# Kernel tuning notes

Measured on AMD Instinct MI355X. Metric: run time of the kernel, lower is better.

## Reference

```python
import jax, jax.numpy as jnp
import numpy as np

HIDDEN = 2048
NUM_HEADS = 8
NUM_KV_HEADS = 1
HEAD_DIM = 256
ROPE_THETA = 10000.0
B, S = 2, 2048


def setup_inputs() -> dict:
    key = jax.random.key(0)
    k1, k2, k3, k4, k5 = jax.random.split(key, 5)
    scale = 0.02
    hidden_states = jax.random.normal(k1, (B, S, HIDDEN), dtype=jnp.float32)
    Wq = jax.random.normal(k2, (HIDDEN, NUM_HEADS * HEAD_DIM), dtype=jnp.float32) * scale
    Wk = jax.random.normal(k3, (HIDDEN, NUM_KV_HEADS * HEAD_DIM), dtype=jnp.float32) * scale
    Wv = jax.random.normal(k4, (HIDDEN, NUM_KV_HEADS * HEAD_DIM), dtype=jnp.float32) * scale
    Wo = jax.random.normal(k5, (NUM_HEADS * HEAD_DIM, HIDDEN), dtype=jnp.float32) * scale
    # causal mask: 1 = attend, 0 = masked (module adds -1e9 where mask==0)
    attention_mask = jnp.tril(jnp.ones((S, S), dtype=jnp.int32))[None, None].repeat(B, axis=0)
    position_ids = jnp.arange(S, dtype=jnp.int32)[None, :].repeat(B, axis=0)
    return {"hidden_states": hidden_states, "Wq": Wq, "Wk": Wk, "Wv": Wv,
            "Wo": Wo, "attention_mask": attention_mask, "position_ids": position_ids}


def _rotate_half(x):
    half = x.shape[-1] // 2
    return jnp.concatenate([-x[..., half:], x[..., :half]], axis=-1)


def _rope_cos_sin(position_ids, head_dim, theta):
    inv_freq = 1.0 / (theta ** (jnp.arange(0, head_dim, 2, dtype=jnp.float32) / head_dim))
    freqs = position_ids.astype(jnp.float32)[:, :, None] * inv_freq[None, None, :]  # [B,S,D/2]
    emb = jnp.concatenate([freqs, freqs], axis=-1)  # [B,S,D]
    return jnp.cos(emb)[:, None], jnp.sin(emb)[:, None]  # [B,1,S,D]


def reference(hidden_states, Wq, Wk, Wv, Wo, attention_mask, position_ids):
    bsz, q_len, _ = hidden_states.shape
    q = (hidden_states @ Wq).reshape(bsz, q_len, NUM_HEADS, HEAD_DIM).transpose(0, 2, 1, 3)
    k = (hidden_states @ Wk).reshape(bsz, q_len, NUM_KV_HEADS, HEAD_DIM).transpose(0, 2, 1, 3)
    v = (hidden_states @ Wv).reshape(bsz, q_len, NUM_KV_HEADS, HEAD_DIM).transpose(0, 2, 1, 3)
    q = q / jnp.sqrt(jnp.float32(HEAD_DIM))  # scale before RoPE, as in source
    cos, sin = _rope_cos_sin(position_ids, HEAD_DIM, ROPE_THETA)
    q = q * cos + _rotate_half(q) * sin
    k = k * cos + _rotate_half(k) * sin
    # GQA: repeat kv heads (prefill: cache == current k,v)
    groups = NUM_HEADS // NUM_KV_HEADS
    k = jnp.repeat(k, groups, axis=1)
    v = jnp.repeat(v, groups, axis=1)
    attn = jnp.einsum('bhqd,bhkd->bhqk', q, k)  # [B,H,S,S]
    additive = jnp.where(attention_mask == 0, jnp.float32(-1e9), jnp.float32(0.0))
    attn = jax.nn.softmax(attn + additive, axis=-1)
    out = jnp.einsum('bhqk,bhkd->bhqd', attn, v)
    out = out.transpose(0, 2, 1, 3).reshape(bsz, q_len, NUM_HEADS * HEAD_DIM)
    out = out @ Wo
    return out, attn
```

## Files before the change

kernel.cpp:

```cpp
#include <hip/hip_runtime.h>

typedef __bf16 bf16_t;
typedef __attribute__((ext_vector_type(4))) float f32x4;
typedef __attribute__((ext_vector_type(8))) __bf16 bf16x8;
typedef __attribute__((ext_vector_type(4))) __bf16 bf16x4;

#define DEVI __device__ __forceinline__

static constexpr int kBsz = 2, kS = 2048, kH = 8, kD = 256, kHid = 2048, kNqkv = 2560;

DEVI void gload_lds16(const void* g, void* l) {
  __builtin_amdgcn_global_load_lds(
      (__attribute__((address_space(1))) unsigned int*)g,
      (__attribute__((address_space(3))) unsigned int*)l, 16, 0, 0);
}

__global__ __launch_bounds__(256) void cast_f32_bf16(const float* __restrict__ in,
                                                     bf16_t* __restrict__ out) {
  int idx = blockIdx.x * 256 + threadIdx.x;
  const float4 f = ((const float4*)in)[idx];
  bf16x4 o;
  o[0] = (bf16_t)f.x; o[1] = (bf16_t)f.y; o[2] = (bf16_t)f.z; o[3] = (bf16_t)f.w;
  ((bf16x4*)out)[idx] = o;
}

__global__ void wtrans_all(const float* __restrict__ Wq, const float* __restrict__ Wk,
                           const float* __restrict__ Wv, const float* __restrict__ Wo,
                           bf16_t* __restrict__ WqkvT, bf16_t* __restrict__ WoT) {
  __shared__ float tile[32][33];
  int zb = blockIdx.x;
  const float* src;
  bf16_t* dst;
  int C, bx, by;
  if (zb < 4096) {
    src = Wq; dst = WqkvT; C = 2048; bx = zb & 63; by = zb >> 6;
  } else if (zb < 4608) {
    int u = zb - 4096; src = Wk; dst = WqkvT + (size_t)2048 * 2048; C = 256; bx = u & 7; by = u >> 3;
  } else if (zb < 5120) {
    int u = zb - 4608; src = Wv; dst = WqkvT + (size_t)2304 * 2048; C = 256; bx = u & 7; by = u >> 3;
  } else {
    int u = zb - 5120; src = Wo; dst = WoT; C = 2048; bx = u & 63; by = u >> 6;
  }
  int c0 = bx * 32, r0 = by * 32;
  int tx = threadIdx.x, ty = threadIdx.y;
#pragma unroll
  for (int k = 0; k < 4; k++)
    tile[ty + 8 * k][tx] = src[(size_t)(r0 + ty + 8 * k) * C + c0 + tx];
  __syncthreads();
#pragma unroll
  for (int k = 0; k < 4; k++)
    dst[(size_t)(c0 + ty + 8 * k) * 2048 + r0 + tx] = (bf16_t)tile[tx][ty + 8 * k];
}

__global__ __launch_bounds__(256) void transpose_v(const bf16_t* __restrict__ qkv,
                                                   bf16_t* __restrict__ vT) {
  __shared__ float tile[32][33];
  int d0 = blockIdx.x * 32, s0 = blockIdx.y * 32, b = blockIdx.z;
  int tx = threadIdx.x, ty = threadIdx.y;
  const bf16_t* in = qkv + ((size_t)(b * kS + s0)) * kNqkv + 2304 + d0;
#pragma unroll
  for (int k = 0; k < 4; k++)
    tile[ty + 8 * k][tx] = (float)in[(size_t)(ty + 8 * k) * kNqkv + tx];
  __syncthreads();
  bf16_t* out = vT + ((size_t)(b * kD + d0)) * kS + s0;
#pragma unroll
  for (int k = 0; k < 4; k++)
    out[(size_t)(ty + 8 * k) * kS + tx] = (bf16_t)tile[tx][ty + 8 * k];
}

__global__ __launch_bounds__(256) void rope_all(const bf16_t* __restrict__ qkv,
                                                const int* __restrict__ pos_ids,
                                                bf16_t* __restrict__ q_bh,
                                                bf16_t* __restrict__ k_b) {
  int bid = blockIdx.x;
  if (bid < 16384) {
    int idx = bid * 256 + threadIdx.x;
    int j = idx & 127, s = (idx >> 7) & 2047, h = (idx >> 18) & 7, b = idx >> 21;
    float invf = exp2f(-0.103810253f * (float)j);
    float ang = (float)pos_ids[b * kS + s] * invf;
    float c, sn;
    sincosf(ang, &sn, &c);
    const bf16_t* src = qkv + ((size_t)(b * kS + s)) * kNqkv + h * kD;
    float x0 = (float)src[j] * 0.0625f;
    float x1 = (float)src[j + 128] * 0.0625f;
    bf16_t* dst = q_bh + ((size_t)((b * kH + h) * kS + s)) * kD;
    dst[j] = (bf16_t)(x0 * c - x1 * sn);
    dst[j + 128] = (bf16_t)(x1 * c + x0 * sn);
  } else {
    int idx = (bid - 16384) * 256 + threadIdx.x;
    int j = idx & 127, s = (idx >> 7) & 2047, b = idx >> 18;
    float invf = exp2f(-0.103810253f * (float)j);
    float ang = (float)pos_ids[b * kS + s] * invf;
    float c, sn;
    sincosf(ang, &sn, &c);
    const bf16_t* src = qkv + ((size_t)(b * kS + s)) * kNqkv + 2048;
    float x0 = (float)src[j];
    float x1 = (float)src[j + 128];
    bf16_t* dst = k_b + ((size_t)(b * kS + s)) * kD;
    dst[j] = (bf16_t)(x0 * c - x1 * sn);
    dst[j + 128] = (bf16_t)(x1 * c + x0 * sn);
  }
}

__global__ __launch_bounds__(256, 4) void attn_fused(
    const bf16_t* __restrict__ q_bh, const bf16_t* __restrict__ k_b,
    float* __restrict__ attn, bf16_t* __restrict__ P) {
  constexpr int KT = 64;
  __shared__ bf16_t ks[KT * 256];
  __shared__ float lstat[64][2];
  __shared__ float rowinv[64];
  const int lin = blockIdx.y * 32 + blockIdx.x;
  const int xr = (lin >> 1) & 31;
  const int flip = (lin ^ (lin >> 8)) & 1;
  const int rt = flip ? 31 - xr : xr;
  const int z = (lin & 1) | (((lin >> 6) & 7) << 1);
  const int b = z >> 3;
  const int nkt = rt + 1, dkt = rt;
  const int m0 = rt * 64;
  const int t = threadIdx.x, lane = t & 63, wv = t >> 6;
  const int wm2 = (wv & 1) * 32, wn2 = (wv >> 1) * 32, wc = wv >> 1;
  const int lrow = lane & 15, quad = lane >> 4;

  bf16x8 qf[2][8];
  {
    const bf16_t* qb = q_bh + ((size_t)z * kS + m0) * kD;
#pragma unroll
    for (int mi = 0; mi < 2; mi++)
#pragma unroll
      for (int k8 = 0; k8 < 8; k8++)
        qf[mi][k8] = *(const bf16x8*)(qb + (size_t)(wm2 + mi * 16 + lrow) * kD + k8 * 32 + quad * 8);
  }
  const bf16_t* kb = k_b + (size_t)b * kS * kD;

  float rs[2][4];
#pragma unroll
  for (int mi = 0; mi < 2; mi++)
#pragma unroll
    for (int rr = 0; rr < 4; rr++) rs[mi][rr] = 0.f;

  for (int kt = 0; kt < nkt; kt++) {
    __syncthreads();
#pragma unroll
    for (int i = 0; i < 8; i++) {
      int slot = i * 256 + t;
      int r = slot >> 5;
      int c = (slot & 31) ^ (r & 7);
      gload_lds16(kb + (size_t)(kt * KT + r) * kD + c * 8, ks + slot * 8);
    }
    __syncthreads();
    f32x4 acc[2][2];
#pragma unroll
    for (int mi = 0; mi < 2; mi++)
#pragma unroll
      for (int ni = 0; ni < 2; ni++) acc[mi][ni] = f32x4{0.f, 0.f, 0.f, 0.f};
    __builtin_amdgcn_s_setprio(1);
#pragma unroll
    for (int k8 = 0; k8 < 8; k8++) {
      bf16x8 bfv[2];
#pragma unroll
      for (int ni = 0; ni < 2; ni++) {
        int R = wn2 + ni * 16 + lrow;
        int c16 = (k8 * 4 + quad) ^ (R & 7);
        bfv[ni] = *(const bf16x8*)(ks + R * 256 + c16 * 8);
      }
#pragma unroll
      for (int mi = 0; mi < 2; mi++)
#pragma unroll
        for (int ni = 0; ni < 2; ni++)
          acc[mi][ni] = __builtin_amdgcn_mfma_f32_16x16x32_bf16(qf[mi][k8], bfv[ni], acc[mi][ni], 0, 0, 0);
    }
    __builtin_amdgcn_s_setprio(0);
    const bool diag = (kt == dkt);
#pragma unroll
    for (int mi = 0; mi < 2; mi++)
#pragma unroll
      for (int rr = 0; rr < 4; rr++) {
        int ml = wm2 + mi * 16 + quad * 4 + rr;
        int mg = m0 + ml;
#pragma unroll
        for (int ni = 0; ni < 2; ni++) {
          int ng = kt * KT + wn2 + ni * 16 + lrow;
          float e = __expf(fminf(acc[mi][ni][rr], 80.f));
          rs[mi][rr] += (!diag || ng <= mg) ? e : 0.f;
        }
      }
  }
#pragma unroll
  for (int mi = 0; mi < 2; mi++)
#pragma unroll
    for (int rr = 0; rr < 4; rr++) {
      float s4 = rs[mi][rr];
      s4 += __shfl_xor(s4, 1); s4 += __shfl_xor(s4, 2);
      s4 += __shfl_xor(s4, 4); s4 += __shfl_xor(s4, 8);
      if (lrow == 0) lstat[wm2 + mi * 16 + quad * 4 + rr][wc] = s4;
    }
  __syncthreads();
  if (t < 64) rowinv[t] = 1.f / (lstat[t][0] + lstat[t][1]);

  float* arow = attn + ((size_t)z * kS + m0) * kS;
  bf16_t* prow = P + ((size_t)z * kS + m0) * kS;
  for (int kt = 0; kt < nkt; kt++) {
    __syncthreads();
#pragma unroll
    for (int i = 0; i < 8; i++) {
      int slot = i * 256 + t;
      int r = slot >> 5;
      int c = (slot & 31) ^ (r & 7);
      gload_lds16(kb + (size_t)(kt * KT + r) * kD + c * 8, ks + slot * 8);
    }
    __syncthreads();
    f32x4 acc[2][2];
#pragma unroll
    for (int mi = 0; mi < 2; mi++)
#pragma unroll
      for (int ni = 0; ni < 2; ni++) acc[mi][ni] = f32x4{0.f, 0.f, 0.f, 0.f};
    __builtin_amdgcn_s_setprio(1);
#pragma unroll
    for (int k8 = 0; k8 < 8; k8++) {
      bf16x8 bfv[2];
#pragma unroll
      for (int ni = 0; ni < 2; ni++) {
        int R = wn2 + ni * 16 + lrow;
        int c16 = (k8 * 4 + quad) ^ (R & 7);
        bfv[ni] = *(const bf16x8*)(ks + R * 256 + c16 * 8);
      }
#pragma unroll
      for (int mi = 0; mi < 2; mi++)
#pragma unroll
        for (int ni = 0; ni < 2; ni++)
          acc[mi][ni] = __builtin_amdgcn_mfma_f32_16x16x32_bf16(qf[mi][k8], bfv[ni], acc[mi][ni], 0, 0, 0);
    }
    __builtin_amdgcn_s_setprio(0);
    const bool diag = (kt == dkt);
#pragma unroll
    for (int mi = 0; mi < 2; mi++)
#pragma unroll
      for (int rr = 0; rr < 4; rr++) {
        int ml = wm2 + mi * 16 + quad * 4 + rr;
        int mg = m0 + ml;
        float inv = rowinv[ml];
        float* ap = arow + (size_t)ml * kS + kt * KT;
        bf16_t* pp = prow + (size_t)ml * kS + kt * KT;
#pragma unroll
        for (int ni = 0; ni < 2; ni++) {
          int nl = wn2 + ni * 16 + lrow;
          int ng = kt * KT + nl;
          float e = __expf(fminf(acc[mi][ni][rr], 80.f)) * inv;
          float pv = (!diag || ng <= mg) ? e : 0.f;
          ap[nl] = pv;
          pp[nl] = (bf16_t)pv;
        }
      }
  }
  int c0 = nkt * KT;
  int nf4 = (kS - c0) >> 2;
  for (int rr = 0; rr < 64; rr++) {
    float* ap = arow + (size_t)rr * kS + c0;
    for (int cc = t; cc < nf4; cc += 256)
      *(float4*)(ap + cc * 4) = make_float4(0.f, 0.f, 0.f, 0.f);
  }
  if ((rt & 1) == 0) {
    int pc0 = nkt * KT;
    int r = t >> 2, cchunk = (t & 3) * 16;
    bf16x8 zz = {(bf16_t)0.f, (bf16_t)0.f, (bf16_t)0.f, (bf16_t)0.f,
                 (bf16_t)0.f, (bf16_t)0.f, (bf16_t)0.f, (bf16_t)0.f};
    *(bf16x8*)(prow + (size_t)r * kS + pc0 + cchunk) = zz;
    *(bf16x8*)(prow + (size_t)r * kS + pc0 + cchunk + 8) = zz;
  }
}

template <int OUT, int CKTR, int BAL = 0>
__global__ __launch_bounds__(256) void gemm_bt(
    const bf16_t* __restrict__ Av, const bf16_t* __restrict__ Btv, void* __restrict__ Cv,
    int K, int lda, int ldb, int ldc,
    long long aBatch, long long bBatch, int bzShift, long long cBatch) {
  constexpr int BM = 128, BN = 128, BK = 64;
  __shared__ bf16_t As[BM * BK];
  __shared__ bf16_t Bs[BN * BK];
  const int z = blockIdx.z;
  const int n0 = blockIdx.x * BN;
  int byi = blockIdx.y;
  if (BAL) {
    if ((blockIdx.x ^ (blockIdx.z >> 3)) & 1) byi = gridDim.y - 1 - byi;
  }
  const int m0 = byi * BM;
  const bf16_t* Bt = Btv + (size_t)(z >> bzShift) * bBatch + (size_t)n0 * ldb;
  const int kEnd = CKTR ? ((m0 + BM < K) ? (m0 + BM) : K) : K;
  const int t = threadIdx.x;
  const int lane = t & 63, wv = t >> 6;
  const int wm = (wv & 1) << 6, wn = (wv >> 1) << 6;
  const int lrow = lane & 15, quad = lane >> 4;
  f32x4 zero = {0.f, 0.f, 0.f, 0.f};
  f32x4 acc[4][4];
#pragma unroll
  for (int i = 0; i < 4; i++)
#pragma unroll
    for (int j = 0; j < 4; j++) acc[i][j] = zero;

  const bf16_t* Ab = Av + (size_t)z * aBatch + (size_t)m0 * lda;

  for (int k0 = 0; k0 < kEnd; k0 += BK) {
    __syncthreads();
#pragma unroll
    for (int i = 0; i < 4; i++) {
      int slot = i * 256 + t;
      int r = slot >> 3, c = slot & 7;
      gload_lds16(Ab + (size_t)r * lda + k0 + c * 8, As + slot * 8);
    }
#pragma unroll
    for (int i = 0; i < 4; i++) {
      int slot = i * 256 + t;
      int r = slot >> 3, c = slot & 7;
      gload_lds16(Bt + (size_t)r * ldb + k0 + c * 8, Bs + slot * 8);
    }
    __syncthreads();
#pragma unroll
    for (int k8 = 0; k8 < 2; k8++) {
      bf16x8 af[4], bfv[4];
#pragma unroll
      for (int i = 0; i < 4; i++)
        af[i] = *(const bf16x8*)(As + (wm + i * 16 + lrow) * BK + k8 * 32 + quad * 8);
#pragma unroll
      for (int i = 0; i < 4; i++)
        bfv[i] = *(const bf16x8*)(Bs + (wn + i * 16 + lrow) * BK + k8 * 32 + quad * 8);
#pragma unroll
      for (int mi = 0; mi < 4; mi++)
#pragma unroll
        for (int ni = 0; ni < 4; ni++)
          acc[mi][ni] = __builtin_amdgcn_mfma_f32_16x16x32_bf16(af[mi], bfv[ni], acc[mi][ni], 0, 0, 0);
    }
  }

  if (OUT == 0) {
    float* C = (float*)Cv + (size_t)z * cBatch;
#pragma unroll
    for (int mi = 0; mi < 4; mi++) {
      int m = m0 + wm + mi * 16 + quad * 4;
#pragma unroll
      for (int ni = 0; ni < 4; ni++) {
        int n = n0 + wn + ni * 16 + lrow;
#pragma unroll
        for (int r = 0; r < 4; r++) C[(size_t)(m + r) * ldc + n] = acc[mi][ni][r];
      }
    }
  } else if (OUT == 1) {
    bf16_t* C = (bf16_t*)Cv + (size_t)(z >> 3) * cBatch + (size_t)(z & 7) * kD;
#pragma unroll
    for (int mi = 0; mi < 4; mi++) {
      int m = m0 + wm + mi * 16 + quad * 4;
#pragma unroll
      for (int ni = 0; ni < 4; ni++) {
        int n = n0 + wn + ni * 16 + lrow;
#pragma unroll
        for (int r = 0; r < 4; r++) C[(size_t)(m + r) * ldc + n] = (bf16_t)acc[mi][ni][r];
      }
    }
  } else {
    bf16_t* C = (bf16_t*)Cv + (size_t)z * cBatch;
#pragma unroll
    for (int mi = 0; mi < 4; mi++) {
      int m = m0 + wm + mi * 16 + quad * 4;
#pragma unroll
      for (int ni = 0; ni < 4; ni++) {
        int n = n0 + wn + ni * 16 + lrow;
#pragma unroll
        for (int r = 0; r < 4; r++) C[(size_t)(m + r) * ldc + n] = (bf16_t)acc[mi][ni][r];
      }
    }
  }
}

extern "C" void kernel_launch(void* const* d_in, const int* in_sizes, int n_in,
                              void* d_out, int out_size, void* d_ws, size_t ws_size,
                              hipStream_t stream) {
  const float* hs = (const float*)d_in[0];
  const float* Wq = (const float*)d_in[1];
  const float* Wk = (const float*)d_in[2];
  const float* Wv = (const float*)d_in[3];
  const float* Wo = (const float*)d_in[4];
  const int* pos = (const int*)d_in[6];

  float* out = (float*)d_out;
  float* attn = out + (size_t)kBsz * kS * kHid;

  char* w = (char*)d_ws;
  bf16_t* hsb = (bf16_t*)w;   w += (size_t)4096 * 2048 * 2;
  bf16_t* WqkvT = (bf16_t*)w; w += (size_t)2560 * 2048 * 2;
  bf16_t* WoT = (bf16_t*)w;   w += (size_t)2048 * 2048 * 2;
  bf16_t* qkv = (bf16_t*)w;   w += (size_t)4096 * 2560 * 2;
  bf16_t* q_bh = (bf16_t*)w;  w += (size_t)8388608 * 2;
  bf16_t* k_b = (bf16_t*)w;   w += (size_t)1048576 * 2;
  bf16_t* vT = (bf16_t*)w;    w += (size_t)1048576 * 2;
  bf16_t* av = (bf16_t*)w;    w += (size_t)8388608 * 2;
  bf16_t* Pb = (bf16_t*)w;    w += (size_t)16 * 2048 * 2048 * 2;

  cast_f32_bf16<<<8192, 256, 0, stream>>>(hs, hsb);
  wtrans_all<<<9216, dim3(32, 8), 0, stream>>>(Wq, Wk, Wv, Wo, WqkvT, WoT);

  gemm_bt<2, 0><<<dim3(20, 32, 1), 256, 0, stream>>>(
      hsb, WqkvT, qkv, 2048, 2048, 2048, 2560, 0, 0, 0, 0);

  rope_all<<<18432, 256, 0, stream>>>(qkv, pos, q_bh, k_b);
  transpose_v<<<dim3(8, 64, 2), dim3(32, 8), 0, stream>>>(qkv, vT);

  attn_fused<<<dim3(32, 16), 256, 0, stream>>>(q_bh, k_b, attn, Pb);

  gemm_bt<1, 1, 1><<<dim3(2, 16, 16), 256, 0, stream>>>(
      Pb, vT, av, 2048, 2048, 2048, 2048,
      (long long)4194304, (long long)524288, 3, (long long)(kS * kHid));

  gemm_bt<0, 0><<<dim3(16, 32, 1), 256, 0, stream>>>(
      av, WoT, out, 2048, 2048, 2048, 2048, 0, 0, 0, 0);
}
```

Measured before the change: 742.1 us.

## Split attention into single-pass unnormalized exp tiles with deferred row normalization

```diff
diff --git a/kernel.cpp b/kernel.cpp
--- a/kernel.cpp
+++ b/kernel.cpp
@@ -22,6 +22,10 @@
   bf16x4 o;
   o[0] = (bf16_t)f.x; o[1] = (bf16_t)f.y; o[2] = (bf16_t)f.z; o[3] = (bf16_t)f.w;
   ((bf16x4*)out)[idx] = o;
+}
+
+__global__ __launch_bounds__(256) void zero_f32(float* __restrict__ p) {
+  p[blockIdx.x * 256 + threadIdx.x] = 0.f;
 }
 
 __global__ void wtrans_all(const float* __restrict__ Wq, const float* __restrict__ Wk,
@@ -102,25 +106,30 @@
   }
 }
 
-__global__ __launch_bounds__(256, 4) void attn_fused(
+__global__ __launch_bounds__(256, 4) void qk_exp(
     const bf16_t* __restrict__ q_bh, const bf16_t* __restrict__ k_b,
-    float* __restrict__ attn, bf16_t* __restrict__ P) {
-  constexpr int KT = 64;
-  __shared__ bf16_t ks[KT * 256];
-  __shared__ float lstat[64][2];
-  __shared__ float rowinv[64];
-  const int lin = blockIdx.y * 32 + blockIdx.x;
-  const int xr = (lin >> 1) & 31;
-  const int flip = (lin ^ (lin >> 8)) & 1;
-  const int rt = flip ? 31 - xr : xr;
-  const int z = (lin & 1) | (((lin >> 6) & 7) << 1);
+    bf16_t* __restrict__ P, float* __restrict__ rowsum) {
+  __shared__ bf16_t ks[64 * 256];
+  const int u = blockIdx.x;
+  const int z = blockIdx.y;
   const int b = z >> 3;
-  const int nkt = rt + 1, dkt = rt;
-  const int m0 = rt * 64;
+  int rt = (int)((sqrtf(8.f * (float)u + 1.f) - 1.f) * 0.5f);
+  while ((rt + 1) * (rt + 2) / 2 <= u) rt++;
+  while (rt * (rt + 1) / 2 > u) rt--;
+  const int kt = u - rt * (rt + 1) / 2;
+  const int m0 = rt * 64, n0 = kt * 64;
   const int t = threadIdx.x, lane = t & 63, wv = t >> 6;
-  const int wm2 = (wv & 1) * 32, wn2 = (wv >> 1) * 32, wc = wv >> 1;
+  const int wm2 = (wv & 1) * 32, wn2 = (wv >> 1) * 32;
   const int lrow = lane & 15, quad = lane >> 4;
 
+  const bf16_t* kb = k_b + (size_t)b * kS * kD;
+#pragma unroll
+  for (int i = 0; i < 8; i++) {
+    int slot = i * 256 + t;
+    int r = slot >> 5;
+    int c = (slot & 31) ^ (r & 7);
+    gload_lds16(kb + (size_t)(n0 + r) * kD + c * 8, ks + slot * 8);
+  }
   bf16x8 qf[2][8];
   {
     const bf16_t* qb = q_bh + ((size_t)z * kS + m0) * kD;
@@ -130,142 +139,94 @@
       for (int k8 = 0; k8 < 8; k8++)
         qf[mi][k8] = *(const bf16x8*)(qb + (size_t)(wm2 + mi * 16 + lrow) * kD + k8 * 32 + quad * 8);
   }
-  const bf16_t* kb = k_b + (size_t)b * kS * kD;
-
-  float rs[2][4];
+  __syncthreads();
+
+  f32x4 acc[2][2];
 #pragma unroll
   for (int mi = 0; mi < 2; mi++)
 #pragma unroll
-    for (int rr = 0; rr < 4; rr++) rs[mi][rr] = 0.f;
-
-  for (int kt = 0; kt < nkt; kt++) {
-    __syncthreads();
-#pragma unroll
-    for (int i = 0; i < 8; i++) {
-      int slot = i * 256 + t;
-      int r = slot >> 5;
-      int c = (slot & 31) ^ (r & 7);
-      gload_lds16(kb + (size_t)(kt * KT + r) * kD + c * 8, ks + slot * 8);
-    }
-    __syncthreads();
-    f32x4 acc[2][2];
+    for (int ni = 0; ni < 2; ni++) acc[mi][ni] = f32x4{0.f, 0.f, 0.f, 0.f};
+  __builtin_amdgcn_s_setprio(1);
+#pragma unroll
+  for (int k8 = 0; k8 < 8; k8++) {
+    bf16x8 bfv[2];
+#pragma unroll
+    for (int ni = 0; ni < 2; ni++) {
+      int R = wn2 + ni * 16 + lrow;
+      int c16 = (k8 * 4 + quad) ^ (R & 7);
+      bfv[ni] = *(const bf16x8*)(ks + R * 256 + c16 * 8);
+    }
 #pragma unroll
     for (int mi = 0; mi < 2; mi++)
 #pragma unroll
-      for (int ni = 0; ni < 2; ni++) acc[mi][ni] = f32x4{0.f, 0.f, 0.f, 0.f};
-    __builtin_amdgcn_s_setprio(1);
-#pragma unroll
-    for (int k8 = 0; k8 < 8; k8++) {
-      bf16x8 bfv[2];
+      for (int ni = 0; ni < 2; ni++)
+        acc[mi][ni] = __builtin_amdgcn_mfma_f32_16x16x32_bf16(qf[mi][k8], bfv[ni], acc[mi][ni], 0, 0, 0);
+  }
+  __builtin_amdgcn_s_setprio(0);
+
+  const bool diag = (kt == rt);
+  bf16_t* pt = P + ((size_t)z * kS + m0) * kS + n0;
+#pragma unroll
+  for (int mi = 0; mi < 2; mi++)
+#pragma unroll
+    for (int rr = 0; rr < 4; rr++) {
+      int ml = wm2 + mi * 16 + quad * 4 + rr;
+      int mg = m0 + ml;
+      float s4 = 0.f;
 #pragma unroll
       for (int ni = 0; ni < 2; ni++) {
-        int R = wn2 + ni * 16 + lrow;
-        int c16 = (k8 * 4 + quad) ^ (R & 7);
-        bfv[ni] = *(const bf16x8*)(ks + R * 256 + c16 * 8);
+        int nl = wn2 + ni * 16 + lrow;
+        int ng = n0 + nl;
+        float e = __expf(fminf(acc[mi][ni][rr], 80.f));
+        bool ok = !diag || ng <= mg;
+        bf16_t pb = ok ? (bf16_t)e : (bf16_t)0.f;
+        pt[(size_t)ml * kS + nl] = pb;
+        s4 += (float)pb;
       }
-#pragma unroll
-      for (int mi = 0; mi < 2; mi++)
-#pragma unroll
-        for (int ni = 0; ni < 2; ni++)
-          acc[mi][ni] = __builtin_amdgcn_mfma_f32_16x16x32_bf16(qf[mi][k8], bfv[ni], acc[mi][ni], 0, 0, 0);
-    }
-    __builtin_amdgcn_s_setprio(0);
-    const bool diag = (kt == dkt);
-#pragma unroll
-    for (int mi = 0; mi < 2; mi++)
-#pragma unroll
-      for (int rr = 0; rr < 4; rr++) {
-        int ml = wm2 + mi * 16 + quad * 4 + rr;
-        int mg = m0 + ml;
-#pragma unroll
-        for (int ni = 0; ni < 2; ni++) {
-          int ng = kt * KT + wn2 + ni * 16 + lrow;
-          float e = __expf(fminf(acc[mi][ni][rr], 80.f));
-          rs[mi][rr] += (!diag || ng <= mg) ? e : 0.f;
-        }
-      }
-  }
-#pragma unroll
-  for (int mi = 0; mi < 2; mi++)
-#pragma unroll
-    for (int rr = 0; rr < 4; rr++) {
-      float s4 = rs[mi][rr];
       s4 += __shfl_xor(s4, 1); s4 += __shfl_xor(s4, 2);
       s4 += __shfl_xor(s4, 4); s4 += __shfl_xor(s4, 8);
-      if (lrow == 0) lstat[wm2 + mi * 16 + quad * 4 + rr][wc] = s4;
-    }
-  __syncthreads();
-  if (t < 64) rowinv[t] = 1.f / (lstat[t][0] + lstat[t][1]);
-
-  float* arow = attn + ((size_t)z * kS + m0) * kS;
-  bf16_t* prow = P + ((size_t)z * kS + m0) * kS;
-  for (int kt = 0; kt < nkt; kt++) {
-    __syncthreads();
-#pragma unroll
-    for (int i = 0; i < 8; i++) {
-      int slot = i * 256 + t;
-      int r = slot >> 5;
-      int c = (slot & 31) ^ (r & 7);
-      gload_lds16(kb + (size_t)(kt * KT + r) * kD + c * 8, ks + slot * 8);
-    }
-    __syncthreads();
-    f32x4 acc[2][2];
-#pragma unroll
-    for (int mi = 0; mi < 2; mi++)
-#pragma unroll
-      for (int ni = 0; ni < 2; ni++) acc[mi][ni] = f32x4{0.f, 0.f, 0.f, 0.f};
-    __builtin_amdgcn_s_setprio(1);
-#pragma unroll
-    for (int k8 = 0; k8 < 8; k8++) {
-      bf16x8 bfv[2];
-#pragma unroll
-      for (int ni = 0; ni < 2; ni++) {
-        int R = wn2 + ni * 16 + lrow;
-        int c16 = (k8 * 4 + quad) ^ (R & 7);
-        bfv[ni] = *(const bf16x8*)(ks + R * 256 + c16 * 8);
-      }
-#pragma unroll
-      for (int mi = 0; mi < 2; mi++)
-#pragma unroll
-        for (int ni = 0; ni < 2; ni++)
-          acc[mi][ni] = __builtin_amdgcn_mfma_f32_16x16x32_bf16(qf[mi][k8], bfv[ni], acc[mi][ni], 0, 0, 0);
-    }
-    __builtin_amdgcn_s_setprio(0);
-    const bool diag = (kt == dkt);
-#pragma unroll
-    for (int mi = 0; mi < 2; mi++)
-#pragma unroll
-      for (int rr = 0; rr < 4; rr++) {
-        int ml = wm2 + mi * 16 + quad * 4 + rr;
-        int mg = m0 + ml;
-        float inv = rowinv[ml];
-        float* ap = arow + (size_t)ml * kS + kt * KT;
-        bf16_t* pp = prow + (size_t)ml * kS + kt * KT;
-#pragma unroll
-        for (int ni = 0; ni < 2; ni++) {
-          int nl = wn2 + ni * 16 + lrow;
-          int ng = kt * KT + nl;
-          float e = __expf(fminf(acc[mi][ni][rr], 80.f)) * inv;
-          float pv = (!diag || ng <= mg) ? e : 0.f;
-          ap[nl] = pv;
-          pp[nl] = (bf16_t)pv;
-        }
-      }
-  }
-  int c0 = nkt * KT;
-  int nf4 = (kS - c0) >> 2;
-  for (int rr = 0; rr < 64; rr++) {
-    float* ap = arow + (size_t)rr * kS + c0;
-    for (int cc = t; cc < nf4; cc += 256)
-      *(float4*)(ap + cc * 4) = make_float4(0.f, 0.f, 0.f, 0.f);
-  }
-  if ((rt & 1) == 0) {
-    int pc0 = nkt * KT;
-    int r = t >> 2, cchunk = (t & 3) * 16;
+      if (lrow == 0) atomicAdd(rowsum + (size_t)z * kS + mg, s4);
+    }
+
+  if (diag && !(rt & 1)) {
     bf16x8 zz = {(bf16_t)0.f, (bf16_t)0.f, (bf16_t)0.f, (bf16_t)0.f,
                  (bf16_t)0.f, (bf16_t)0.f, (bf16_t)0.f, (bf16_t)0.f};
-    *(bf16x8*)(prow + (size_t)r * kS + pc0 + cchunk) = zz;
-    *(bf16x8*)(prow + (size_t)r * kS + pc0 + cchunk + 8) = zz;
+    int r = t >> 2, cc = (t & 3) * 16;
+    bf16_t* pz = P + ((size_t)z * kS + m0 + r) * kS + n0 + 64 + cc;
+    *(bf16x8*)pz = zz;
+    *(bf16x8*)(pz + 8) = zz;
+  }
+}
+
+__global__ __launch_bounds__(256) void attn_expand(
+    const bf16_t* __restrict__ P, const float* __restrict__ rowsum,
+    float* __restrict__ attn) {
+  const int rt = blockIdx.y, z = blockIdx.z;
+  const int m0 = rt * 64;
+  const int t = threadIdx.x;
+  const int r = t >> 2;
+  const int cbase = blockIdx.x * 512 + (t & 3) * 8;
+  const int ncaus = (rt + 1) * 64;
+  const float inv = 1.f / rowsum[(size_t)z * kS + m0 + r];
+  const size_t rowoff = ((size_t)z * kS + m0 + r) * kS;
+  const bf16_t* pr = P + rowoff;
+  float* ar = attn + rowoff;
+#pragma unroll
+  for (int it = 0; it < 16; it++) {
+    int col = cbase + it * 32;
+    float4 o0, o1;
+    if (col < ncaus) {
+      bf16x8 pv = *(const bf16x8*)(pr + col);
+      o0 = make_float4((float)pv[0] * inv, (float)pv[1] * inv,
+                       (float)pv[2] * inv, (float)pv[3] * inv);
+      o1 = make_float4((float)pv[4] * inv, (float)pv[5] * inv,
+                       (float)pv[6] * inv, (float)pv[7] * inv);
+    } else {
+      o0 = make_float4(0.f, 0.f, 0.f, 0.f);
+      o1 = o0;
+    }
+    *(float4*)(ar + col) = o0;
+    *(float4*)(ar + col + 4) = o1;
   }
 }
 
@@ -273,7 +234,8 @@
 __global__ __launch_bounds__(256) void gemm_bt(
     const bf16_t* __restrict__ Av, const bf16_t* __restrict__ Btv, void* __restrict__ Cv,
     int K, int lda, int ldb, int ldc,
-    long long aBatch, long long bBatch, int bzShift, long long cBatch) {
+    long long aBatch, long long bBatch, int bzShift, long long cBatch,
+    const float* __restrict__ rowsum) {
   constexpr int BM = 128, BN = 128, BK = 64;
   __shared__ bf16_t As[BM * BK];
   __shared__ bf16_t Bs[BN * BK];
@@ -348,11 +310,15 @@
 #pragma unroll
     for (int mi = 0; mi < 4; mi++) {
       int m = m0 + wm + mi * 16 + quad * 4;
+      float inv[4];
+#pragma unroll
+      for (int r = 0; r < 4; r++) inv[r] = 1.f / rowsum[(size_t)z * kS + m + r];
 #pragma unroll
       for (int ni = 0; ni < 4; ni++) {
         int n = n0 + wn + ni * 16 + lrow;
 #pragma unroll
-        for (int r = 0; r < 4; r++) C[(size_t)(m + r) * ldc + n] = (bf16_t)acc[mi][ni][r];
+        for (int r = 0; r < 4; r++)
+          C[(size_t)(m + r) * ldc + n] = (bf16_t)(acc[mi][ni][r] * inv[r]);
       }
     }
   } else {
@@ -393,22 +359,26 @@
   bf16_t* vT = (bf16_t*)w;    w += (size_t)1048576 * 2;
   bf16_t* av = (bf16_t*)w;    w += (size_t)8388608 * 2;
   bf16_t* Pb = (bf16_t*)w;    w += (size_t)16 * 2048 * 2048 * 2;
+  float* rowsum = (float*)w;  w += (size_t)16 * 2048 * 4;
 
   cast_f32_bf16<<<8192, 256, 0, stream>>>(hs, hsb);
   wtrans_all<<<9216, dim3(32, 8), 0, stream>>>(Wq, Wk, Wv, Wo, WqkvT, WoT);
+  zero_f32<<<128, 256, 0, stream>>>(rowsum);
 
   gemm_bt<2, 0><<<dim3(20, 32, 1), 256, 0, stream>>>(
-      hsb, WqkvT, qkv, 2048, 2048, 2048, 2560, 0, 0, 0, 0);
+      hsb, WqkvT, qkv, 2048, 2048, 2048, 2560, 0, 0, 0, 0, nullptr);
 
   rope_all<<<18432, 256, 0, stream>>>(qkv, pos, q_bh, k_b);
   transpose_v<<<dim3(8, 64, 2), dim3(32, 8), 0, stream>>>(qkv, vT);
 
-  attn_fused<<<dim3(32, 16), 256, 0, stream>>>(q_bh, k_b, attn, Pb);
+  qk_exp<<<dim3(528, 16), 256, 0, stream>>>(q_bh, k_b, Pb, rowsum);
+
+  attn_expand<<<dim3(4, 32, 16), 256, 0, stream>>>(Pb, rowsum, attn);
 
   gemm_bt<1, 1, 1><<<dim3(2, 16, 16), 256, 0, stream>>>(
       Pb, vT, av, 2048, 2048, 2048, 2048,
-      (long long)4194304, (long long)524288, 3, (long long)(kS * kHid));
+      (long long)4194304, (long long)524288, 3, (long long)(kS * kHid), rowsum);
 
   gemm_bt<0, 0><<<dim3(16, 32, 1), 256, 0, stream>>>(
-      av, WoT, out, 2048, 2048, 2048, 2048, 0, 0, 0, 0);
-}
+      av, WoT, out, 2048, 2048, 2048, 2048, 0, 0, 0, 0, nullptr);
+}
```

New measurement: 740.3 us. No clear change (-0.2%).
